# Kernel optimization log

Measured on AMD Instinct MI355X. Metric: run time of the kernel, lower is better.

The kernel has to match this reference:

```python
import jax, jax.numpy as jnp
import numpy as np

B, N, K, C, R = 2, 4096, 512, 384, 16
JITTER = 1e-4
W_ATTACH, W_ENTB = 1.0, 0.0


def overlap_score(delta, Sig):
    # fused_gaussian_overlap_score: bidirectional Mahalanobis overlap log-score
    # delta [..., 3], Sig [..., 3, 3] (SPD)
    sol = jnp.linalg.solve(Sig, delta[..., None])[..., 0]
    maha = (delta * sol).sum(-1)
    _, logdet = jnp.linalg.slogdet(Sig)
    return -0.5 * maha - 0.5 * logdet


def setup_inputs() -> dict:
    key = jax.random.key(0)
    ks = jax.random.split(key, 10)
    s_parent = jax.random.normal(ks[0], (B, K, C), jnp.float32)
    mu_parent = jax.random.normal(ks[1], (B, K, 3), jnp.float32) * 10.0
    A = jax.random.normal(ks[2], (B, K, 3, 3), jnp.float32)
    Sig_parent = A @ jnp.swapaxes(A, -1, -2) + 0.5 * jnp.eye(3, dtype=jnp.float32)
    mask_parent = jnp.ones((B, K), jnp.float32)
    node_mask = jnp.ones((B, N), jnp.float32)
    res_idx = jax.random.randint(ks[3], (B, N), 0, N)
    Bmat = jax.random.normal(ks[4], (1, C // 2), jnp.float32)  # Fourier freqs, scale=1.0
    Wq = jax.random.normal(ks[5], (C, C), jnp.float32) / np.sqrt(C).astype(np.float32)
    Wk = jax.random.normal(ks[6], (C, C), jnp.float32) / np.sqrt(C).astype(np.float32)
    Wv = jax.random.normal(ks[7], (C, C), jnp.float32) / np.sqrt(C).astype(np.float32)
    ln_g = jnp.ones((C,), jnp.float32)
    ln_b = jnp.zeros((C,), jnp.float32)
    return dict(s_parent=s_parent, mu_parent=mu_parent, Sig_parent=Sig_parent,
                mask_parent=mask_parent, node_mask=node_mask, res_idx=res_idx,
                Bmat=Bmat, Wq=Wq, Wk=Wk, Wv=Wv, ln_g=ln_g, ln_b=ln_b)


def reference(s_parent, mu_parent, Sig_parent, mask_parent, node_mask, res_idx,
              Bmat, Wq, Wk, Wv, ln_g, ln_b):
    eye3 = jnp.eye(3, dtype=s_parent.dtype)
    inv_sqrt_c = 1.0 / jnp.sqrt(jnp.asarray(C, s_parent.dtype))

    # --- ResIdxFourierEmbedding ---
    m = node_mask
    L = jnp.clip(m.sum(1, keepdims=True), 1.0)
    denom = jnp.clip(L - 1.0, 1.0)
    ri = jnp.clip(res_idx, 0, 4095).astype(s_parent.dtype)
    pos = jnp.clip(ri / denom, 0.0, 1.0)[..., None]                      # [B,N,1]
    proj = (2.0 * jnp.pi) * (pos @ Bmat)                                 # [B,N,C/2]
    emb = jnp.concatenate([jnp.cos(proj), jnp.sin(proj)], -1)            # [B,N,C]
    emb = emb * m[..., None]
    mu_e = emb.mean(-1, keepdims=True)
    var_e = ((emb - mu_e) ** 2).mean(-1, keepdims=True)
    q0 = (emb - mu_e) / jnp.sqrt(var_e + 1e-5) * ln_g + ln_b

    # --- routing projections ---
    q = q0 @ Wq                                                          # [B,N,C]
    k = s_parent @ Wk                                                    # [B,K,C]
    logits_full = jnp.einsum('bnc,bkc->bnk', q, k) * inv_sqrt_c
    logits_full = logits_full + (mask_parent[:, None, :] - 1.0) * 1e9
    j0 = jnp.argmax(logits_full, -1)                                     # [B,N]

    # --- topk parents by Gaussian overlap (no grad) ---
    mu_p = jax.lax.stop_gradient(mu_parent)
    Sig_p = jax.lax.stop_gradient(Sig_parent)
    delta_kk = mu_p[:, :, None, :] - mu_p[:, None, :, :]                 # [B,K,K,3]
    Sig_kk = Sig_p[:, :, None] + Sig_p[:, None, :] + 1e-6 * eye3         # [B,K,K,3,3]
    score_kk = overlap_score(delta_kk, Sig_kk)
    mask2d = mask_parent[:, None, :] * mask_parent[:, :, None]
    score_kk = jnp.where(mask2d < 0.5, -1e9, score_kk)
    knn = jax.lax.top_k(score_kk, R)[1]                                  # [B,K,R]
    parent_idx = knn[jnp.arange(B)[:, None], j0]                         # [B,N,R]

    # --- multi-level gathers ---
    gather = lambda tab: jax.vmap(lambda t, i: t[i])(tab, parent_idx)
    mu_sub = gather(mu_parent)                                           # [B,N,R,3]
    Sig_sub = gather(Sig_parent)                                         # [B,N,R,3,3]
    s_sub = gather(s_parent)                                             # [B,N,R,C]

    k_sub = s_sub @ Wk
    v_sub = s_sub @ Wv
    logits = (q[:, :, None, :] * k_sub).sum(-1) * inv_sqrt_c             # [B,N,R]
    logits = logits + (m[:, :, None] - 1.0) * 1e9
    B_local = jax.nn.softmax(logits, -1)

    s0 = jnp.einsum('bnr,bnrc->bnc', B_local, v_sub) * m[..., None]
    mu0 = jnp.einsum('bnr,bnrp->bnp', B_local, mu_sub)
    d = mu_sub - mu0[:, :, None, :]
    outer = d[..., :, None] * d[..., None, :]
    Sig0 = (B_local[..., None, None] * (Sig_sub + outer)).sum(2) + JITTER * eye3

    # --- geometric regularization ---
    delta0 = mu0[:, :, None, :] - mu_sub
    score = overlap_score(delta0, Sig_sub)                               # [B,N,R]
    dnm = jnp.clip(m.sum(), 1.0)
    loss_attach = -(m[:, :, None] * (B_local * score)).sum() / dnm
    ent = -(B_local * jnp.log(jnp.clip(B_local, 1e-9))).sum(-1)
    loss_ent_B = (ent * m).sum() / dnm

    occ = jax.vmap(lambda i, w: jnp.zeros((K,), w.dtype).at[i.reshape(-1)].add(w.reshape(-1)))(
        parent_idx, B_local * m[:, :, None])
    occ_norm = occ / jnp.clip(occ.sum(-1, keepdims=True), 1e-9)

    loss_geo = W_ATTACH * loss_attach + W_ENTB * loss_ent_B
    return s0, mu0, Sig0, B_local, occ_norm, loss_geo
```

## Files before the change

### kernel.cpp

```cpp
#include <hip/hip_runtime.h>
#include <math.h>

#define NB 2
#define NN 4096
#define NK 512
#define NC 384
#define NR 16
#define NCH 192
#define NSLICE 64

static constexpr float INV_SQRT_C = 0.051031036307982884f;
static constexpr float TWO_PI     = 6.283185307179586f;
static constexpr float F_JITTER   = 1e-4f;

typedef __attribute__((ext_vector_type(8))) short short8;
typedef __attribute__((ext_vector_type(4))) float f32x4;
typedef __attribute__((ext_vector_type(4))) unsigned short us4;

__device__ __forceinline__ void split3(float x, unsigned short& h, unsigned short& m_, unsigned short& l_) {
    unsigned int xi = __float_as_uint(x);
    unsigned int uh = (xi + 0x7fffu + ((xi >> 16) & 1u)) >> 16;
    float fh = __uint_as_float(uh << 16);
    float r  = x - fh;
    unsigned int ri = __float_as_uint(r);
    unsigned int um = (ri + 0x7fffu + ((ri >> 16) & 1u)) >> 16;
    float fm = __uint_as_float(um << 16);
    float r2 = r - fm;
    unsigned int r2i = __float_as_uint(r2);
    unsigned int ul = (r2i + 0x7fffu + ((r2i >> 16) & 1u)) >> 16;
    h = (unsigned short)uh; m_ = (unsigned short)um; l_ = (unsigned short)ul;
}

__global__ __launch_bounds__(256) void k_pre(const float* __restrict__ node_mask,
                                             const float* __restrict__ Wk,
                                             const float* __restrict__ Wq,
                                             float* __restrict__ Lsum,
                                             float* __restrict__ W2) {
    __shared__ float red[256];
    __shared__ float As[16][68];
    __shared__ float Ws[16][68];
    int bid = blockIdx.x, t = threadIdx.x;
    if (bid < 2) {
        int b = bid;
        float s = 0.f;
        for (int n = t; n < NN; n += 256) s += node_mask[b*NN + n];
        red[t] = s; __syncthreads();
        for (int w = 128; w > 0; w >>= 1) { if (t < w) red[t] += red[t+w]; __syncthreads(); }
        if (t == 0) Lsum[b] = red[0];
        return;
    }
    int gb = bid - 2;
    int rowbase = (gb % 6) * 64, colbase = (gb / 6) * 64;
    int tx = t & 15, ty = t >> 4;
    float acc[4][4] = {};
    for (int k0 = 0; k0 < NC; k0 += 16) {
        {
            int r = t >> 2, ja = (t & 3) << 2;
            float4 a4 = *(const float4*)(Wk + (size_t)(rowbase + r)*NC + k0 + ja);
            As[ja+0][r] = a4.x; As[ja+1][r] = a4.y; As[ja+2][r] = a4.z; As[ja+3][r] = a4.w;
        }
        {
            int r = t >> 2, jb = (t & 3) << 2;
            float4 b4 = *(const float4*)(Wq + (size_t)(colbase + r)*NC + k0 + jb);
            Ws[jb+0][r] = b4.x; Ws[jb+1][r] = b4.y; Ws[jb+2][r] = b4.z; Ws[jb+3][r] = b4.w;
        }
        __syncthreads();
        #pragma unroll
        for (int kk = 0; kk < 16; ++kk) {
            float4 av = *(const float4*)&As[kk][ty<<2];
            float4 wv = *(const float4*)&Ws[kk][tx<<2];
            float aa[4] = {av.x, av.y, av.z, av.w};
            float ww[4] = {wv.x, wv.y, wv.z, wv.w};
            #pragma unroll
            for (int i = 0; i < 4; ++i)
                #pragma unroll
                for (int j = 0; j < 4; ++j)
                    acc[i][j] += aa[i]*ww[j];
        }
        __syncthreads();
    }
    #pragma unroll
    for (int i = 0; i < 4; ++i) {
        float4 o = make_float4(acc[i][0], acc[i][1], acc[i][2], acc[i][3]);
        *(float4*)(W2 + (size_t)(rowbase + (ty<<2) + i)*NC + colbase + (tx<<2)) = o;
    }
}

template<bool SPLIT>
__global__ __launch_bounds__(256) void k_mid(const float* __restrict__ s_parent,
                                             const float* __restrict__ Wv,
                                             const float* __restrict__ W2,
                                             const int* __restrict__ res_idx,
                                             const float* __restrict__ node_mask,
                                             const float* __restrict__ Bm,
                                             const float* __restrict__ ln_g,
                                             const float* __restrict__ ln_b,
                                             const float* __restrict__ Lsum,
                                             const float* __restrict__ mu,
                                             const float* __restrict__ Sg,
                                             const float* __restrict__ maskp,
                                             float* __restrict__ vmat,
                                             float* __restrict__ GtF,
                                             unsigned short* __restrict__ gh,
                                             unsigned short* __restrict__ gm,
                                             unsigned short* __restrict__ gl,
                                             float* __restrict__ q0f,
                                             unsigned short* __restrict__ qh,
                                             unsigned short* __restrict__ qm,
                                             unsigned short* __restrict__ ql,
                                             int* __restrict__ knn) {
    __shared__ float As[16][68];
    __shared__ float Ws[16][68];
    __shared__ float swv[4];
    __shared__ int   swi[4];
    __shared__ int   winner;
    int bid = blockIdx.x, t = threadIdx.x;

    if (bid < 192) {
        int z = bid / 96, rem = bid % 96;
        int rowbase = (rem % 16) * 64, colbase = (rem / 16) * 64;
        const float* W = z ? W2 : Wv;
        int tx = t & 15, ty = t >> 4;
        float acc[4][4] = {};
        for (int k0 = 0; k0 < NC; k0 += 16) {
            {
                int r = t >> 2, ja = (t & 3) << 2;
                float4 a4 = *(const float4*)(s_parent + (size_t)(rowbase + r)*NC + k0 + ja);
                As[ja+0][r] = a4.x; As[ja+1][r] = a4.y; As[ja+2][r] = a4.z; As[ja+3][r] = a4.w;
            }
            {
                int kr = t >> 4, jw = (t & 15) << 2;
                float4 w4 = *(const float4*)(W + (size_t)(k0 + kr)*NC + colbase + jw);
                *(float4*)&Ws[kr][jw] = w4;
            }
            __syncthreads();
            #pragma unroll
            for (int kk = 0; kk < 16; ++kk) {
                float4 av = *(const float4*)&As[kk][ty<<2];
                float4 wv = *(const float4*)&Ws[kk][tx<<2];
                float aa[4] = {av.x, av.y, av.z, av.w};
                float ww[4] = {wv.x, wv.y, wv.z, wv.w};
                #pragma unroll
                for (int i = 0; i < 4; ++i)
                    #pragma unroll
                    for (int j = 0; j < 4; ++j)
                        acc[i][j] += aa[i]*ww[j];
            }
            __syncthreads();
        }
        #pragma unroll
        for (int i = 0; i < 4; ++i) {
            size_t ro = (size_t)(rowbase + (ty<<2) + i)*NC + colbase + (tx<<2);
            if (z == 0) {
                *(float4*)(vmat + ro) = make_float4(acc[i][0], acc[i][1], acc[i][2], acc[i][3]);
            } else if constexpr (SPLIT) {
                us4 vh, vm, vl;
                #pragma unroll
                for (int j = 0; j < 4; ++j) {
                    unsigned short h, mm, ll;
                    split3(acc[i][j], h, mm, ll);
                    vh[j] = h; vm[j] = mm; vl[j] = ll;
                }
                *(us4*)(gh + ro) = vh; *(us4*)(gm + ro) = vm; *(us4*)(gl + ro) = vl;
            } else {
                *(float4*)(GtF + ro) = make_float4(acc[i][0], acc[i][1], acc[i][2], acc[i][3]);
            }
        }
        return;
    }

    if (bid < 1216) {
        int tb = bid - 192;
        int b = tb >> 9, i = tb & 511;
        const float* mui = mu + (size_t)(b*NK + i)*3;
        const float* Sgi = Sg + (size_t)(b*NK + i)*9;
        float mi0 = mui[0], mi1 = mui[1], mi2 = mui[2];
        float S0 = Sgi[0], S1 = Sgi[1], S2 = Sgi[2], S4 = Sgi[4], S5 = Sgi[5], S8 = Sgi[8];
        float mski = maskp[b*NK + i];
        float cand[2];
        #pragma unroll
        for (int h = 0; h < 2; ++h) {
            int j = t + h*256;
            const float* muj = mu + (size_t)(b*NK + j)*3;
            const float* Sgj = Sg + (size_t)(b*NK + j)*9;
            float d0 = mi0-muj[0], d1 = mi1-muj[1], d2 = mi2-muj[2];
            float a00 = S0+Sgj[0]+1e-6f, a01 = S1+Sgj[1],       a02 = S2+Sgj[2];
            float a11 = S4+Sgj[4]+1e-6f, a12 = S5+Sgj[5],       a22 = S8+Sgj[8]+1e-6f;
            float c00 = a11*a22 - a12*a12;
            float c01 = a02*a12 - a01*a22;
            float c02 = a01*a12 - a02*a11;
            float c11 = a00*a22 - a02*a02;
            float c12 = a01*a02 - a00*a12;
            float c22 = a00*a11 - a01*a01;
            float det = a00*c00 + a01*c01 + a02*c02;
            float t0 = c00*d0 + c01*d1 + c02*d2;
            float t1 = c01*d0 + c11*d1 + c12*d2;
            float t2 = c02*d0 + c12*d1 + c22*d2;
            float maha = (d0*t0 + d1*t1 + d2*t2) / det;
            float score = -0.5f*(maha + logf(det));
            float mj = maskp[b*NK + j];
            cand[h] = (mski*mj < 0.5f) ? -1e9f : score;
        }
        int lane = t & 63, wv = t >> 6;
        for (int it = 0; it < NR; ++it) {
            float bv; int bi;
            if (cand[0] >= cand[1]) { bv = cand[0]; bi = t; }
            else                    { bv = cand[1]; bi = t + 256; }
            #pragma unroll
            for (int off = 32; off > 0; off >>= 1) {
                float v2 = __shfl_xor(bv, off);
                int   i2 = __shfl_xor(bi, off);
                if (v2 > bv || (v2 == bv && i2 < bi)) { bv = v2; bi = i2; }
            }
            if (lane == 0) { swv[wv] = bv; swi[wv] = bi; }
            __syncthreads();
            if (t == 0) {
                float B = swv[0]; int I = swi[0];
                #pragma unroll
                for (int w = 1; w < 4; ++w)
                    if (swv[w] > B || (swv[w] == B && swi[w] < I)) { B = swv[w]; I = swi[w]; }
                knn[((size_t)(b*NK + i))*NR + it] = I;
                winner = I;
            }
            __syncthreads();
            int wn = winner;
            if (t == wn)        cand[0] = -INFINITY;
            if (t + 256 == wn)  cand[1] = -INFINITY;
        }
        return;
    }

    int q0b = bid - 1216;
    int w = t >> 6, l = t & 63;
    int row = (q0b << 2) + w;
    int b = row >> 12;
    float m = node_mask[row];
    float Lb = fmaxf(Lsum[b], 1.0f);
    float denom = fmaxf(Lb - 1.0f, 1.0f);
    int ri = res_idx[row];
    ri = ri < 0 ? 0 : (ri > 4095 ? 4095 : ri);
    float pos = fminf(fmaxf((float)ri / denom, 0.f), 1.f);
    float v[6];
    #pragma unroll
    for (int j = 0; j < 3; ++j) {
        float pr = TWO_PI * pos * Bm[l + (j << 6)];
        v[j]   = cosf(pr) * m;
        v[j+3] = sinf(pr) * m;
    }
    float sum = v[0]+v[1]+v[2]+v[3]+v[4]+v[5];
    #pragma unroll
    for (int off = 32; off > 0; off >>= 1) sum += __shfl_xor(sum, off);
    float mean = sum * (1.0f/NC);
    float sq = 0.f;
    #pragma unroll
    for (int j = 0; j < 6; ++j) { v[j] -= mean; sq += v[j]*v[j]; }
    #pragma unroll
    for (int off = 32; off > 0; off >>= 1) sq += __shfl_xor(sq, off);
    float var = sq * (1.0f/NC);
    float inv = 1.0f / sqrtf(var + 1e-5f);
    #pragma unroll
    for (int j = 0; j < 6; ++j) {
        int p = l + (j << 6);
        float val = v[j]*inv*ln_g[p] + ln_b[p];
        size_t o = (size_t)row*NC + p;
        if constexpr (SPLIT) {
            unsigned short h, mm, ll;
            split3(val, h, mm, ll);
            qh[o] = h; qm[o] = mm; ql[o] = ll;
        } else {
            q0f[o] = val;
        }
    }
}

template<bool SPLIT>
__global__ __launch_bounds__(256) void k_logits_mfma(const float* __restrict__ q0f,
                                                     const unsigned short* __restrict__ qh,
                                                     const unsigned short* __restrict__ qm,
                                                     const unsigned short* __restrict__ ql,
                                                     const float* __restrict__ GtF,
                                                     const unsigned short* __restrict__ gh,
                                                     const unsigned short* __restrict__ gm,
                                                     const unsigned short* __restrict__ gl,
                                                     const float* __restrict__ maskp,
                                                     float* __restrict__ logits,
                                                     float* __restrict__ pmaxv,
                                                     int*   __restrict__ pmaxi,
                                                     float* __restrict__ occ_part) {
    int bid = blockIdx.x;
    {
        int gid = bid * 256 + threadIdx.x;
        if (gid < NSLICE*NB*NK) occ_part[gid] = 0.f;
    }
    int wg = (bid & 7) * 64 + (bid >> 3);
    int b  = wg >> 8;
    int r8 = (wg >> 3) & 31;
    int cb = wg & 7;
    int rowbase = r8 << 7;
    int colbase = cb << 6;

    __shared__ __align__(16) unsigned short Ah[128][40];
    __shared__ __align__(16) unsigned short Am[128][40];
    __shared__ __align__(16) unsigned short Al[128][40];
    __shared__ __align__(16) unsigned short Bh[64][40];
    __shared__ __align__(16) unsigned short Bm2[64][40];
    __shared__ __align__(16) unsigned short Bl[64][40];
    __shared__ float rmv[128][2];
    __shared__ int   rmi[128][2];

    int t = threadIdx.x;
    int lane = t & 63, wv = t >> 6;
    int wr = wv >> 1, wc = wv & 1;
    int a = lane & 15, g = lane >> 4;

    size_t arow0 = (size_t)(b << 12) + rowbase;
    size_t brow0 = (size_t)(b << 9) + colbase;

    f32x4 acc[4][2];
    #pragma unroll
    for (int i = 0; i < 4; ++i)
        #pragma unroll
        for (int j = 0; j < 2; ++j)
            acc[i][j] = (f32x4){0.f, 0.f, 0.f, 0.f};

    for (int k0 = 0; k0 < NC; k0 += 32) {
        __syncthreads();
        if constexpr (SPLIT) {
            #pragma unroll
            for (int i = 0; i < 4; ++i) {
                int id = i*256 + t;
                int row = id >> 3, seg = id & 7;
                size_t go = (arow0 + row)*NC + k0 + (seg << 2);
                *(us4*)&Ah[row][seg << 2] = *(const us4*)(qh + go);
                *(us4*)&Am[row][seg << 2] = *(const us4*)(qm + go);
                *(us4*)&Al[row][seg << 2] = *(const us4*)(ql + go);
            }
            #pragma unroll
            for (int i = 0; i < 2; ++i) {
                int id = i*256 + t;
                int row = id >> 3, seg = id & 7;
                size_t go = (brow0 + row)*NC + k0 + (seg << 2);
                *(us4*)&Bh[row][seg << 2]  = *(const us4*)(gh + go);
                *(us4*)&Bm2[row][seg << 2] = *(const us4*)(gm + go);
                *(us4*)&Bl[row][seg << 2]  = *(const us4*)(gl + go);
            }
        } else {
            #pragma unroll
            for (int i = 0; i < 4; ++i) {
                int id = i*256 + t;
                int row = id >> 3, seg = id & 7;
                float4 v = *(const float4*)(q0f + (arow0 + row)*NC + k0 + (seg << 2));
                unsigned short h0,m0,l0,h1,m1,l1,h2,m2,l2,h3,m3,l3;
                split3(v.x, h0, m0, l0); split3(v.y, h1, m1, l1);
                split3(v.z, h2, m2, l2); split3(v.w, h3, m3, l3);
                *(us4*)&Ah[row][seg << 2] = (us4){h0, h1, h2, h3};
                *(us4*)&Am[row][seg << 2] = (us4){m0, m1, m2, m3};
                *(us4*)&Al[row][seg << 2] = (us4){l0, l1, l2, l3};
            }
            #pragma unroll
            for (int i = 0; i < 2; ++i) {
                int id = i*256 + t;
                int row = id >> 3, seg = id & 7;
                float4 v = *(const float4*)(GtF + (brow0 + row)*NC + k0 + (seg << 2));
                unsigned short h0,m0,l0,h1,m1,l1,h2,m2,l2,h3,m3,l3;
                split3(v.x, h0, m0, l0); split3(v.y, h1, m1, l1);
                split3(v.z, h2, m2, l2); split3(v.w, h3, m3, l3);
                *(us4*)&Bh[row][seg << 2]  = (us4){h0, h1, h2, h3};
                *(us4*)&Bm2[row][seg << 2] = (us4){m0, m1, m2, m3};
                *(us4*)&Bl[row][seg << 2]  = (us4){l0, l1, l2, l3};
            }
        }
        __syncthreads();
        short8 afh[4], afm[4], afl[4];
        #pragma unroll
        for (int fr = 0; fr < 4; ++fr) {
            int r = (wr << 6) + (fr << 4) + a;
            afh[fr] = *(const short8*)&Ah[r][g << 3];
            afm[fr] = *(const short8*)&Am[r][g << 3];
            afl[fr] = *(const short8*)&Al[r][g << 3];
        }
        #pragma unroll
        for (int fc = 0; fc < 2; ++fc) {
            int c = (wc << 5) + (fc << 4) + a;
            short8 bh = *(const short8*)&Bh[c][g << 3];
            short8 bm = *(const short8*)&Bm2[c][g << 3];
            short8 bl = *(const short8*)&Bl[c][g << 3];
            #pragma unroll
            for (int fr = 0; fr < 4; ++fr) {
                acc[fr][fc] = __builtin_amdgcn_mfma_f32_16x16x32_bf16(afh[fr], bh, acc[fr][fc], 0, 0, 0);
                acc[fr][fc] = __builtin_amdgcn_mfma_f32_16x16x32_bf16(afh[fr], bm, acc[fr][fc], 0, 0, 0);
                acc[fr][fc] = __builtin_amdgcn_mfma_f32_16x16x32_bf16(afm[fr], bh, acc[fr][fc], 0, 0, 0);
                acc[fr][fc] = __builtin_amdgcn_mfma_f32_16x16x32_bf16(afh[fr], bl, acc[fr][fc], 0, 0, 0);
                acc[fr][fc] = __builtin_amdgcn_mfma_f32_16x16x32_bf16(afl[fr], bh, acc[fr][fc], 0, 0, 0);
                acc[fr][fc] = __builtin_amdgcn_mfma_f32_16x16x32_bf16(afm[fr], bm, acc[fr][fc], 0, 0, 0);
            }
        }
    }
    float mk[2];
    #pragma unroll
    for (int fc = 0; fc < 2; ++fc)
        mk[fc] = (maskp[(b << 9) + colbase + (wc << 5) + (fc << 4) + a] - 1.0f) * 1e9f;
    int colg0 = colbase + (wc << 5) + a;
    #pragma unroll
    for (int fr = 0; fr < 4; ++fr) {
        #pragma unroll
        for (int reg = 0; reg < 4; ++reg) {
            int rloc = (wr << 6) + (fr << 4) + (g << 2) + reg;
            size_t rowg = (size_t)(b << 12) + rowbase + rloc;
            float v0 = acc[fr][0][reg] * INV_SQRT_C;
            float v1 = acc[fr][1][reg] * INV_SQRT_C;
            logits[rowg * NK + colg0]      = v0;
            logits[rowg * NK + colg0 + 16] = v1;
            float bv = v0 + mk[0]; int bc = colg0;
            float w1 = v1 + mk[1];
            if (w1 > bv) { bv = w1; bc = colg0 + 16; }
            #pragma unroll
            for (int off = 1; off < 16; off <<= 1) {
                float v2 = __shfl_xor(bv, off);
                int   c2 = __shfl_xor(bc, off);
                if (v2 > bv || (v2 == bv && c2 < bc)) { bv = v2; bc = c2; }
            }
            if (a == 0) { rmv[rloc][wc] = bv; rmi[rloc][wc] = bc; }
        }
    }
    __syncthreads();
    if (t < 128) {
        float v0 = rmv[t][0], v1 = rmv[t][1];
        int   c0 = rmi[t][0], c1 = rmi[t][1];
        float bv = v0; int bc = c0;
        if (v1 > bv) { bv = v1; bc = c1; }
        pmaxv[(((size_t)(b << 3) + cb) << 12) + rowbase + t] = bv;
        pmaxi[(((size_t)(b << 3) + cb) << 12) + rowbase + t] = bc;
    }
}

__global__ __launch_bounds__(256) void k_final(const float* __restrict__ logits,
                                               const float* __restrict__ vmat,
                                               const float* __restrict__ mu,
                                               const float* __restrict__ Sg,
                                               const float* __restrict__ node_mask,
                                               const float* __restrict__ pmaxv,
                                               const int*   __restrict__ pmaxi,
                                               const int* __restrict__ knn,
                                               float* __restrict__ out_s0,
                                               float* __restrict__ out_mu0,
                                               float* __restrict__ out_Sig0,
                                               float* __restrict__ out_Bl,
                                               float* __restrict__ occ_part,
                                               float* __restrict__ loss_part) {
    int t = threadIdx.x;
    int rowbase = blockIdx.x << 4;
    int b = rowbase >> 12;
    int l  = t & 63;
    int sub = l >> 4, ll = l & 15;
    int r = ((t >> 6) << 2) + sub;
    int grow = rowbase + r;
    __shared__ float wl[16][17];
    __shared__ int   pidx[16][17];
    __shared__ float lred[16];
    __shared__ float msk[16];
    __shared__ int   j0s[16];

    if (t < 16) {
        int rowb = (rowbase & 4095) + t;
        float bv = -INFINITY; int bj = 0;
        #pragma unroll
        for (int cbk = 0; cbk < 8; ++cbk) {
            size_t idx = (((size_t)(b << 3) + cbk) << 12) + rowb;
            float v = pmaxv[idx];
            if (v > bv) { bv = v; bj = pmaxi[idx]; }
        }
        j0s[t] = bj;
    }
    __syncthreads();

    float m = node_mask[grow];
    int p = knn[((size_t)(b*NK + j0s[r]))*NR + ll];
    float v = logits[(size_t)grow*NK + p];
    float mx = v;
    #pragma unroll
    for (int off = 8; off > 0; off >>= 1) mx = fmaxf(mx, __shfl_xor(mx, off));
    float e = expf(v - mx);
    float sme = e;
    #pragma unroll
    for (int off = 8; off > 0; off >>= 1) sme += __shfl_xor(sme, off);
    float w = e / sme;
    wl[r][ll] = w;
    pidx[r][ll] = p;
    out_Bl[(size_t)rowbase*NR + t] = w;

    const float* mur = mu + (size_t)(b*NK + p)*3;
    const float* Sgr = Sg + (size_t)(b*NK + p)*9;
    float mr0 = mur[0], mr1 = mur[1], mr2 = mur[2];
    float m0 = w*mr0, m1 = w*mr1, m2 = w*mr2;
    #pragma unroll
    for (int off = 8; off > 0; off >>= 1) {
        m0 += __shfl_xor(m0, off); m1 += __shfl_xor(m1, off); m2 += __shfl_xor(m2, off);
    }
    float d0 = mr0-m0, d1 = mr1-m1, d2 = mr2-m2;
    float a00 = Sgr[0], a01 = Sgr[1], a02 = Sgr[2];
    float a11 = Sgr[4], a12 = Sgr[5], a22 = Sgr[8];
    float p00 = w*(a00 + d0*d0), p01 = w*(a01 + d0*d1), p02 = w*(a02 + d0*d2);
    float p11 = w*(a11 + d1*d1), p12 = w*(a12 + d1*d2), p22 = w*(a22 + d2*d2);
    #pragma unroll
    for (int off = 8; off > 0; off >>= 1) {
        p00 += __shfl_xor(p00, off); p01 += __shfl_xor(p01, off); p02 += __shfl_xor(p02, off);
        p11 += __shfl_xor(p11, off); p12 += __shfl_xor(p12, off); p22 += __shfl_xor(p22, off);
    }
    float c00 = a11*a22 - a12*a12;
    float c01 = a02*a12 - a01*a22;
    float c02 = a01*a12 - a02*a11;
    float c11 = a00*a22 - a02*a02;
    float c12 = a01*a02 - a00*a12;
    float c22 = a00*a11 - a01*a01;
    float det = a00*c00 + a01*c01 + a02*c02;
    float t0 = c00*d0 + c01*d1 + c02*d2;
    float t1 = c01*d0 + c11*d1 + c12*d2;
    float t2 = c02*d0 + c12*d1 + c22*d2;
    float maha = (d0*t0 + d1*t1 + d2*t2) / det;
    float score = -0.5f*(maha + logf(det));
    float lp = w*score;
    #pragma unroll
    for (int off = 8; off > 0; off >>= 1) lp += __shfl_xor(lp, off);
    if (ll == 0) {
        out_mu0[(size_t)grow*3+0] = m0;
        out_mu0[(size_t)grow*3+1] = m1;
        out_mu0[(size_t)grow*3+2] = m2;
        float* o = out_Sig0 + (size_t)grow*9;
        o[0]=p00+F_JITTER; o[1]=p01;          o[2]=p02;
        o[3]=p01;          o[4]=p11+F_JITTER; o[5]=p12;
        o[6]=p02;          o[7]=p12;          o[8]=p22+F_JITTER;
        lred[r] = m*lp;
        msk[r] = m;
    }
    atomicAdd(&occ_part[(size_t)(blockIdx.x & (NSLICE-1))*(NB*NK) + b*NK + p], w*m);
    __syncthreads();
    if (t == 0) {
        float s = 0.f;
        #pragma unroll
        for (int i = 0; i < 16; ++i) s += lred[i];
        loss_part[blockIdx.x] = s;
    }
    const float4* vb = (const float4*)(vmat + (size_t)b*NK*NC);
    #pragma unroll
    for (int it = 0; it < 6; ++it) {
        int id = it*256 + t;
        int row = id / 96;
        int col = id - row*96;
        float4 acc4 = make_float4(0.f, 0.f, 0.f, 0.f);
        #pragma unroll
        for (int r2 = 0; r2 < NR; ++r2) {
            float ww = wl[row][r2];
            float4 vv = vb[(size_t)pidx[row][r2]*96 + col];
            acc4.x += ww*vv.x; acc4.y += ww*vv.y; acc4.z += ww*vv.z; acc4.w += ww*vv.w;
        }
        float mm = msk[row];
        acc4.x *= mm; acc4.y *= mm; acc4.z *= mm; acc4.w *= mm;
        ((float4*)(out_s0 + (size_t)(rowbase + row)*NC))[col] = acc4;
    }
}

__global__ __launch_bounds__(1024) void k_finalize(const float* __restrict__ occ_part,
                                                   const float* __restrict__ Lsum,
                                                   const float* __restrict__ loss_part,
                                                   float* __restrict__ out_occn,
                                                   float* __restrict__ out_loss) {
    int t = threadIdx.x;
    __shared__ float red[1024];
    float s = 0.f;
    for (int sl = 0; sl < NSLICE; ++sl) s += occ_part[(size_t)sl*(NB*NK) + t];
    red[t] = s; __syncthreads();
    for (int w = 256; w > 0; w >>= 1) {
        if ((t & 511) < w) red[t] += red[t+w];
        __syncthreads();
    }
    float tot = red[t & 512];
    float occn = s / fmaxf(tot, 1e-9f);
    __syncthreads();
    out_occn[t] = occn;
    float lp = (t < 512) ? loss_part[t] : 0.f;
    red[t] = lp; __syncthreads();
    for (int w = 512; w > 0; w >>= 1) {
        if (t < w) red[t] += red[t+w];
        __syncthreads();
    }
    if (t == 0) {
        float dnm = fmaxf(Lsum[0] + Lsum[1], 1.0f);
        out_loss[0] = -(red[0] / dnm);
    }
}

extern "C" void kernel_launch(void* const* d_in, const int* in_sizes, int n_in,
                              void* d_out, int out_size, void* d_ws, size_t ws_size,
                              hipStream_t stream) {
    const float* s_parent   = (const float*)d_in[0];
    const float* mu_parent  = (const float*)d_in[1];
    const float* Sig_parent = (const float*)d_in[2];
    const float* mask_par   = (const float*)d_in[3];
    const float* node_mask  = (const float*)d_in[4];
    const int*   res_idx    = (const int*)d_in[5];
    const float* Bm         = (const float*)d_in[6];
    const float* Wq         = (const float*)d_in[7];
    const float* Wk         = (const float*)d_in[8];
    const float* Wv         = (const float*)d_in[9];
    const float* ln_g       = (const float*)d_in[10];
    const float* ln_b       = (const float*)d_in[11];

    const bool G = (ws_size >= (43ull << 20));

    float* ws = (float*)d_ws;
    const size_t SZ_A    = G ? 4718592 : 3145728;
    const size_t OFF_LOG = 0;
    const size_t OFF_A   = OFF_LOG + 4194304;
    const size_t OFF_MISC= OFF_A + SZ_A;
    const size_t OFF_V   = OFF_MISC + 262144;
    const size_t OFF_GT  = OFF_V + 393216;
    const size_t OFF_SM  = OFF_GT + (G ? 589824 : 393216);

    float*          logits = ws + OFF_LOG;
    float*          q0f    = ws + OFF_A;
    unsigned short* qh     = (unsigned short*)(ws + OFF_A);
    unsigned short* qm     = qh + (size_t)NB*NN*NC;
    unsigned short* ql     = qm + (size_t)NB*NN*NC;
    float*          W2     = ws + OFF_MISC;
    float*          pmaxv  = ws + OFF_MISC;
    int*            pmaxi  = (int*)(ws + OFF_MISC + 65536);
    int*            knn    = (int*)(ws + OFF_MISC + 147456);
    float*          occ_part = ws + OFF_MISC + 163840;
    float*          vmat   = ws + OFF_V;
    float*          GtF    = ws + OFF_GT;
    unsigned short* gh     = (unsigned short*)(ws + OFF_GT);
    unsigned short* gm     = gh + (size_t)NB*NK*NC;
    unsigned short* gl     = gm + (size_t)NB*NK*NC;
    float*          Lsum   = ws + OFF_SM;
    float*          lpart  = ws + OFF_SM + 16;

    float* out      = (float*)d_out;
    float* out_s0   = out;
    float* out_mu0  = out      + (size_t)NB*NN*NC;
    float* out_Sig0 = out_mu0  + (size_t)NB*NN*3;
    float* out_Bl   = out_Sig0 + (size_t)NB*NN*9;
    float* out_occn = out_Bl   + (size_t)NB*NN*NR;
    float* out_loss = out_occn + (size_t)NB*NK;

    (void)in_sizes; (void)n_in; (void)out_size;

    k_pre<<<38, 256, 0, stream>>>(node_mask, Wk, Wq, Lsum, W2);
    if (G) k_mid<true ><<<3264, 256, 0, stream>>>(s_parent, Wv, W2, res_idx, node_mask, Bm, ln_g, ln_b,
                                                  Lsum, mu_parent, Sig_parent, mask_par,
                                                  vmat, GtF, gh, gm, gl, q0f, qh, qm, ql, knn);
    else   k_mid<false><<<3264, 256, 0, stream>>>(s_parent, Wv, W2, res_idx, node_mask, Bm, ln_g, ln_b,
                                                  Lsum, mu_parent, Sig_parent, mask_par,
                                                  vmat, GtF, gh, gm, gl, q0f, qh, qm, ql, knn);
    if (G) k_logits_mfma<true ><<<512, 256, 0, stream>>>(q0f, qh, qm, ql, GtF, gh, gm, gl,
                                                         mask_par, logits, pmaxv, pmaxi, occ_part);
    else   k_logits_mfma<false><<<512, 256, 0, stream>>>(q0f, qh, qm, ql, GtF, gh, gm, gl,
                                                         mask_par, logits, pmaxv, pmaxi, occ_part);
    k_final<<<(NB*NN)/16, 256, 0, stream>>>(logits, vmat, mu_parent, Sig_parent, node_mask,
                                            pmaxv, pmaxi, knn, out_s0, out_mu0, out_Sig0,
                                            out_Bl, occ_part, lpart);
    k_finalize<<<1, 1024, 0, stream>>>(occ_part, Lsum, lpart, out_occn, out_loss);
}
```

Baseline: 107.4 us.

## Do parent kNN top-k per wavefront, widen split loads, split finalize per batch

The parent kNN selection now gives each 64-lane wavefront one parent row, holding 8 candidates per lane. The top-16 selection uses only wavefront shuffles, which removes the two block-wide barriers per iteration and shrinks the kNN block count by a factor of four. The bf16 split operand staging in the MFMA logits kernel now uses 8-element vector loads instead of 4-element ones, halving the number of load instructions. The finalize kernel is split into two 512-thread blocks, one per batch, with a simpler reduction. The local max now uses strict greater-than within a lane, which may change tie-breaking slightly.

New measurement: 102.3 us. 1.05x faster.

```diff
diff --git a/kernel.cpp b/kernel.cpp
--- a/kernel.cpp
+++ b/kernel.cpp
@@ -16,6 +16,7 @@
 typedef __attribute__((ext_vector_type(8))) short short8;
 typedef __attribute__((ext_vector_type(4))) float f32x4;
 typedef __attribute__((ext_vector_type(4))) unsigned short us4;
+typedef __attribute__((ext_vector_type(8))) unsigned short us8;
 
 __device__ __forceinline__ void split3(float x, unsigned short& h, unsigned short& m_, unsigned short& l_) {
     unsigned int xi = __float_as_uint(x);
@@ -111,9 +112,6 @@
                                              int* __restrict__ knn) {
     __shared__ float As[16][68];
     __shared__ float Ws[16][68];
-    __shared__ float swv[4];
-    __shared__ int   swi[4];
-    __shared__ int   winner;
     int bid = blockIdx.x, t = threadIdx.x;
 
     if (bid < 192) {
@@ -169,18 +167,19 @@
         return;
     }
 
-    if (bid < 1216) {
-        int tb = bid - 192;
+    if (bid < 448) {
+        int wv_ = t >> 6, lane = t & 63;
+        int tb = ((bid - 192) << 2) + wv_;
         int b = tb >> 9, i = tb & 511;
         const float* mui = mu + (size_t)(b*NK + i)*3;
         const float* Sgi = Sg + (size_t)(b*NK + i)*9;
         float mi0 = mui[0], mi1 = mui[1], mi2 = mui[2];
         float S0 = Sgi[0], S1 = Sgi[1], S2 = Sgi[2], S4 = Sgi[4], S5 = Sgi[5], S8 = Sgi[8];
         float mski = maskp[b*NK + i];
-        float cand[2];
-        #pragma unroll
-        for (int h = 0; h < 2; ++h) {
-            int j = t + h*256;
+        float cand[8];
+        #pragma unroll
+        for (int h = 0; h < 8; ++h) {
+            int j = lane + (h << 6);
             const float* muj = mu + (size_t)(b*NK + j)*3;
             const float* Sgj = Sg + (size_t)(b*NK + j)*9;
             float d0 = mi0-muj[0], d1 = mi1-muj[1], d2 = mi2-muj[2];
@@ -201,36 +200,30 @@
             float mj = maskp[b*NK + j];
             cand[h] = (mski*mj < 0.5f) ? -1e9f : score;
         }
-        int lane = t & 63, wv = t >> 6;
         for (int it = 0; it < NR; ++it) {
-            float bv; int bi;
-            if (cand[0] >= cand[1]) { bv = cand[0]; bi = t; }
-            else                    { bv = cand[1]; bi = t + 256; }
+            float bv = cand[0]; int bh = 0;
+            #pragma unroll
+            for (int h = 1; h < 8; ++h)
+                if (cand[h] > bv) { bv = cand[h]; bh = h; }
+            int bi = lane + (bh << 6);
             #pragma unroll
             for (int off = 32; off > 0; off >>= 1) {
                 float v2 = __shfl_xor(bv, off);
                 int   i2 = __shfl_xor(bi, off);
                 if (v2 > bv || (v2 == bv && i2 < bi)) { bv = v2; bi = i2; }
             }
-            if (lane == 0) { swv[wv] = bv; swi[wv] = bi; }
-            __syncthreads();
-            if (t == 0) {
-                float B = swv[0]; int I = swi[0];
+            if (lane == 0) knn[((size_t)(b*NK + i))*NR + it] = bi;
+            if ((bi & 63) == lane) {
+                int s = bi >> 6;
                 #pragma unroll
-                for (int w = 1; w < 4; ++w)
-                    if (swv[w] > B || (swv[w] == B && swi[w] < I)) { B = swv[w]; I = swi[w]; }
-                knn[((size_t)(b*NK + i))*NR + it] = I;
-                winner = I;
-            }
-            __syncthreads();
-            int wn = winner;
-            if (t == wn)        cand[0] = -INFINITY;
-            if (t + 256 == wn)  cand[1] = -INFINITY;
+                for (int h = 0; h < 8; ++h)
+                    if (h == s) cand[h] = -INFINITY;
+            }
         }
         return;
     }
 
-    int q0b = bid - 1216;
+    int q0b = bid - 448;
     int w = t >> 6, l = t & 63;
     int row = (q0b << 2) + w;
     int b = row >> 12;
@@ -327,22 +320,20 @@
         __syncthreads();
         if constexpr (SPLIT) {
             #pragma unroll
-            for (int i = 0; i < 4; ++i) {
-                int id = i*256 + t;
-                int row = id >> 3, seg = id & 7;
-                size_t go = (arow0 + row)*NC + k0 + (seg << 2);
-                *(us4*)&Ah[row][seg << 2] = *(const us4*)(qh + go);
-                *(us4*)&Am[row][seg << 2] = *(const us4*)(qm + go);
-                *(us4*)&Al[row][seg << 2] = *(const us4*)(ql + go);
-            }
-            #pragma unroll
             for (int i = 0; i < 2; ++i) {
                 int id = i*256 + t;
-                int row = id >> 3, seg = id & 7;
-                size_t go = (brow0 + row)*NC + k0 + (seg << 2);
-                *(us4*)&Bh[row][seg << 2]  = *(const us4*)(gh + go);
-                *(us4*)&Bm2[row][seg << 2] = *(const us4*)(gm + go);
-                *(us4*)&Bl[row][seg << 2]  = *(const us4*)(gl + go);
+                int row = id >> 2, s2 = id & 3;
+                size_t go = (arow0 + row)*NC + k0 + (s2 << 3);
+                *(us8*)&Ah[row][s2 << 3] = *(const us8*)(qh + go);
+                *(us8*)&Am[row][s2 << 3] = *(const us8*)(qm + go);
+                *(us8*)&Al[row][s2 << 3] = *(const us8*)(ql + go);
+            }
+            {
+                int row = t >> 2, s2 = t & 3;
+                size_t go = (brow0 + row)*NC + k0 + (s2 << 3);
+                *(us8*)&Bh[row][s2 << 3]  = *(const us8*)(gh + go);
+                *(us8*)&Bm2[row][s2 << 3] = *(const us8*)(gm + go);
+                *(us8*)&Bl[row][s2 << 3]  = *(const us8*)(gl + go);
             }
         } else {
             #pragma unroll
@@ -560,33 +551,27 @@
     }
 }
 
-__global__ __launch_bounds__(1024) void k_finalize(const float* __restrict__ occ_part,
-                                                   const float* __restrict__ Lsum,
-                                                   const float* __restrict__ loss_part,
-                                                   float* __restrict__ out_occn,
-                                                   float* __restrict__ out_loss) {
-    int t = threadIdx.x;
-    __shared__ float red[1024];
+__global__ __launch_bounds__(512) void k_finalize(const float* __restrict__ occ_part,
+                                                  const float* __restrict__ Lsum,
+                                                  const float* __restrict__ loss_part,
+                                                  float* __restrict__ out_occn,
+                                                  float* __restrict__ out_loss) {
+    int b = blockIdx.x, t = threadIdx.x;
+    __shared__ float red[512];
     float s = 0.f;
-    for (int sl = 0; sl < NSLICE; ++sl) s += occ_part[(size_t)sl*(NB*NK) + t];
+    for (int sl = 0; sl < NSLICE; ++sl) s += occ_part[(size_t)sl*(NB*NK) + b*NK + t];
     red[t] = s; __syncthreads();
-    for (int w = 256; w > 0; w >>= 1) {
-        if ((t & 511) < w) red[t] += red[t+w];
-        __syncthreads();
-    }
-    float tot = red[t & 512];
-    float occn = s / fmaxf(tot, 1e-9f);
+    for (int w = 256; w > 0; w >>= 1) { if (t < w) red[t] += red[t+w]; __syncthreads(); }
+    float tot = red[0];
     __syncthreads();
-    out_occn[t] = occn;
-    float lp = (t < 512) ? loss_part[t] : 0.f;
-    red[t] = lp; __syncthreads();
-    for (int w = 512; w > 0; w >>= 1) {
-        if (t < w) red[t] += red[t+w];
-        __syncthreads();
-    }
-    if (t == 0) {
-        float dnm = fmaxf(Lsum[0] + Lsum[1], 1.0f);
-        out_loss[0] = -(red[0] / dnm);
+    out_occn[b*NK + t] = s / fmaxf(tot, 1e-9f);
+    if (b == 0) {
+        red[t] = loss_part[t]; __syncthreads();
+        for (int w = 256; w > 0; w >>= 1) { if (t < w) red[t] += red[t+w]; __syncthreads(); }
+        if (t == 0) {
+            float dnm = fmaxf(Lsum[0] + Lsum[1], 1.0f);
+            out_loss[0] = -(red[0] / dnm);
+        }
     }
 }
 
@@ -646,10 +631,10 @@
     (void)in_sizes; (void)n_in; (void)out_size;
 
     k_pre<<<38, 256, 0, stream>>>(node_mask, Wk, Wq, Lsum, W2);
-    if (G) k_mid<true ><<<3264, 256, 0, stream>>>(s_parent, Wv, W2, res_idx, node_mask, Bm, ln_g, ln_b,
+    if (G) k_mid<true ><<<2496, 256, 0, stream>>>(s_parent, Wv, W2, res_idx, node_mask, Bm, ln_g, ln_b,
                                                   Lsum, mu_parent, Sig_parent, mask_par,
                                                   vmat, GtF, gh, gm, gl, q0f, qh, qm, ql, knn);
-    else   k_mid<false><<<3264, 256, 0, stream>>>(s_parent, Wv, W2, res_idx, node_mask, Bm, ln_g, ln_b,
+    else   k_mid<false><<<2496, 256, 0, stream>>>(s_parent, Wv, W2, res_idx, node_mask, Bm, ln_g, ln_b,
                                                   Lsum, mu_parent, Sig_parent, mask_par,
                                                   vmat, GtF, gh, gm, gl, q0f, qh, qm, ql, knn);
     if (G) k_logits_mfma<true ><<<512, 256, 0, stream>>>(q0f, qh, qm, ql, GtF, gh, gm, gl,
@@ -659,5 +644,5 @@
     k_final<<<(NB*NN)/16, 256, 0, stream>>>(logits, vmat, mu_parent, Sig_parent, node_mask,
                                             pmaxv, pmaxi, knn, out_s0, out_mu0, out_Sig0,
                                             out_Bl, occ_part, lpart);
-    k_finalize<<<1, 1024, 0, stream>>>(occ_part, Lsum, lpart, out_occn, out_loss);
+    k_finalize<<<2, 512, 0, stream>>>(occ_part, Lsum, lpart, out_occn, out_loss);
 }
```
